# Optimization experiments

Hardware: AMD Instinct MI355X
Metric: run time of the kernel (lower is better)

Reference implementation:

```python
import jax, jax.numpy as jnp
import numpy as np

B, S, HID = 2, 2048, 2048
H, DH = 16, 128
SCALE = 1.0 / np.sqrt(DH)


def setup_inputs() -> dict:
    key = jax.random.key(0)
    ks = jax.random.split(key, 5)
    std = 1.0 / np.sqrt(HID)
    return {
        "x": jax.random.normal(ks[0], (B, S, HID), dtype=jnp.float32),
        "wq": jax.random.normal(ks[1], (HID, HID), dtype=jnp.float32) * std,
        "wk": jax.random.normal(ks[2], (HID, HID), dtype=jnp.float32) * std,
        "wv": jax.random.normal(ks[3], (HID, HID), dtype=jnp.float32) * std,
        "wo": jax.random.normal(ks[4], (HID, HID), dtype=jnp.float32) * std,
    }


def reference(x, wq, wk, wv, wo):
    # nn.Linear(h, h, bias=False): y = x @ W^T
    q = (x @ wq.T).reshape(B, S, H, DH).transpose(0, 2, 1, 3)  # [B,H,S,Dh]
    k = (x @ wk.T).reshape(B, S, H, DH).transpose(0, 2, 1, 3)
    v = (x @ wv.T).reshape(B, S, H, DH).transpose(0, 2, 1, 3)
    scores = jnp.einsum("bhsd,bhtd->bhst", q, k) * SCALE  # [B,H,S,S]
    attn = jax.nn.softmax(scores.astype(jnp.float32), axis=-1).astype(q.dtype)
    # dropout p=0.0 (eval): identity
    out = jnp.einsum("bhst,bhtd->bhsd", attn, v)  # [B,H,S,Dh]
    out = out.transpose(0, 2, 1, 3).reshape(B, S, HID)
    return out @ wo.T
```

## Files before the change

kernel.cpp:

```cpp
#include <hip/hip_runtime.h>
#include <hip/hip_bf16.h>
#include <stdint.h>

typedef __attribute__((ext_vector_type(8))) short short8;
typedef __attribute__((ext_vector_type(4))) short short4v;
typedef __attribute__((ext_vector_type(4))) float f32x4;
typedef __attribute__((ext_vector_type(4))) unsigned int uint4v;

static __device__ __forceinline__ ushort f2bf(float f) {
    uint32_t u = __builtin_bit_cast(uint32_t, f);
    uint32_t r = (u + 0x7FFFu + ((u >> 16) & 1u)) >> 16;
    return (ushort)r;
}

static __device__ __forceinline__ uint32_t cvt_pk_bf16(float lo, float hi) {
    uint32_t d;
    asm("v_cvt_pk_bf16_f32 %0, %1, %2" : "=v"(d) : "v"(lo), "v"(hi));
    return d;
}

static __device__ __forceinline__ void async_copy16(const void* g, void* l) {
    __builtin_amdgcn_global_load_lds(
        (const __attribute__((address_space(1))) uint32_t*)g,
        (__attribute__((address_space(3))) uint32_t*)l, 16, 0, 0);
}

#define TR16(P3, IMM)                                                        \
    ({                                                                       \
        short4v _d;                                                          \
        asm volatile("ds_read_b64_tr_b16 %0, %1 offset:" #IMM                \
                     : "=v"(_d) : "v"(P3));                                  \
        _d;                                                                  \
    })

#define CAT8(a, b) __builtin_shufflevector(a, b, 0, 1, 2, 3, 4, 5, 6, 7)

__global__ __launch_bounds__(256) void cast_kernel(const float* __restrict__ in,
                                                   ushort* __restrict__ out, int n4) {
    int i = blockIdx.x * 256 + threadIdx.x;
    if (i >= n4) return;
    float4 v = reinterpret_cast<const float4*>(in)[i];
    uint2 o;
    o.x = cvt_pk_bf16(v.x, v.y);
    o.y = cvt_pk_bf16(v.z, v.w);
    reinterpret_cast<uint2*>(out)[i] = o;
}

__global__ __launch_bounds__(256) void cast3_kernel(const float* __restrict__ a,
                                                    const float* __restrict__ b,
                                                    const float* __restrict__ c,
                                                    ushort* __restrict__ out, int n4each) {
    int i = blockIdx.x * 256 + threadIdx.x;
    int which = i / n4each;
    int j = i - which * n4each;
    const float* src = which == 0 ? a : (which == 1 ? b : c);
    if (which > 2) return;
    float4 v = reinterpret_cast<const float4*>(src)[j];
    uint2 o;
    o.x = cvt_pk_bf16(v.x, v.y);
    o.y = cvt_pk_bf16(v.z, v.w);
    reinterpret_cast<uint2*>(out)[i] = o;
}

static __device__ __forceinline__ void store_val(float* C, size_t idx, float v) { C[idx] = v; }
static __device__ __forceinline__ void store_val(ushort* C, size_t idx, float v) { C[idx] = f2bf(v); }

template <typename OutT>
__global__ __launch_bounds__(256) void gemm_bt_kernel(const ushort* __restrict__ A,
                                                      const ushort* __restrict__ B,
                                                      OutT* __restrict__ C,
                                                      int M, int N, int K) {
    __shared__ __align__(16) ushort As[128 * 32];
    __shared__ __align__(16) ushort Bs[128 * 32];
    const int tid = threadIdx.x;
    const int w = tid >> 6, lane = tid & 63;
    const int fr = lane & 15, fq = lane >> 4;
    const int wr = w >> 1, wc = w & 1;
    const int bpn = N >> 7;
    const int which = blockIdx.x / bpn;
    const int row0 = blockIdx.y * 128;
    const int gcol0 = blockIdx.x * 128;
    const int col0 = gcol0 - which * N;
    OutT* Cw = C + (size_t)which * M * N;

    const int srow = tid >> 2;
    const int scol = (tid & 3) * 8;
    const ushort* ga0 = A + (size_t)(row0 + srow) * K + scol;
    const ushort* ga1 = A + (size_t)(row0 + 64 + srow) * K + scol;
    const ushort* gb0 = B + (size_t)(gcol0 + srow) * K + scol;
    const ushort* gb1 = B + (size_t)(gcol0 + 64 + srow) * K + scol;
    ushort* la0 = &As[(w * 64) * 8];
    ushort* la1 = &As[(256 + w * 64) * 8];
    ushort* lb0 = &Bs[(w * 64) * 8];
    ushort* lb1 = &Bs[(256 + w * 64) * 8];

    f32x4 acc[4][4];
#pragma unroll
    for (int m = 0; m < 4; ++m)
#pragma unroll
        for (int n = 0; n < 4; ++n) acc[m][n] = f32x4{0.f, 0.f, 0.f, 0.f};

    for (int kt = 0; kt < K; kt += 32) {
        __syncthreads();
        async_copy16(ga0 + kt, la0);
        async_copy16(ga1 + kt, la1);
        async_copy16(gb0 + kt, lb0);
        async_copy16(gb1 + kt, lb1);
        __syncthreads();
        short8 af[4], bfr[4];
#pragma unroll
        for (int m = 0; m < 4; ++m)
            af[m] = *(const short8*)&As[(wr * 64 + m * 16 + fr) * 32 + fq * 8];
#pragma unroll
        for (int n = 0; n < 4; ++n)
            bfr[n] = *(const short8*)&Bs[(wc * 64 + n * 16 + fr) * 32 + fq * 8];
#pragma unroll
        for (int m = 0; m < 4; ++m)
#pragma unroll
            for (int n = 0; n < 4; ++n)
                acc[m][n] = __builtin_amdgcn_mfma_f32_16x16x32_bf16(af[m], bfr[n], acc[m][n], 0, 0, 0);
    }

#pragma unroll
    for (int m = 0; m < 4; ++m) {
        const int grow = row0 + wr * 64 + m * 16 + fq * 4;
#pragma unroll
        for (int n = 0; n < 4; ++n) {
            const int gcol = col0 + wc * 64 + n * 16 + fr;
#pragma unroll
            for (int r = 0; r < 4; ++r)
                store_val(Cw, (size_t)(grow + r) * N + gcol, acc[m][n][r]);
        }
    }
}

__global__ __launch_bounds__(512) void attn_kernel(const ushort* __restrict__ Q,
                                                   const ushort* __restrict__ K,
                                                   const ushort* __restrict__ V,
                                                   ushort* __restrict__ O,
                                                   int S, int HID, float scale) {
    __shared__ __align__(16) ushort Ks[64 * 128];
    __shared__ __align__(16) ushort Vs[64 * 128];

    const int tid = threadIdx.x, w = tid >> 6, lane = tid & 63;
    const int fr = lane & 15, fq = lane >> 4;
    const int qt = blockIdx.x, h = blockIdx.y, b = blockIdx.z;
    const size_t rs = (size_t)HID;
    const int qr0 = qt * 128 + w * 16;
    const float c1 = scale * 1.4426950408889634f;

    short8 qf[4];
    {
        const ushort* qp = Q + ((size_t)(b * S) + qr0 + fr) * rs + h * 128 + fq * 8;
#pragma unroll
        for (int ks = 0; ks < 4; ++ks) qf[ks] = *(const short8*)(qp + ks * 32);
    }

    f32x4 of[8];
#pragma unroll
    for (int n = 0; n < 8; ++n) of[n] = f32x4{0.f, 0.f, 0.f, 0.f};
    float m2 = -1e30f;
    float l = 0.f;

    const ushort* Kb = K + (size_t)(b * S) * rs + h * 128;
    const ushort* Vb = V + (size_t)(b * S) * rs + h * 128;

    size_t koff[2];
#pragma unroll
    for (int j = 0; j < 2; ++j) {
        int row = j * 32 + w * 4 + (lane >> 4);
        int colb = ((lane & 15) * 16) ^ ((row & 7) << 4);
        koff[j] = (size_t)row * rs + (colb >> 1);
    }
    size_t voff[2];
#pragma unroll
    for (int j = 0; j < 2; ++j) {
        int L = j * 64 + w * 8 + (lane >> 3);
        int kv = (L >> 3) * 4 + ((lane >> 1) & 3);
        int dh = (L & 7) * 16 + (lane & 1) * 8;
        voff[j] = (size_t)kv * rs + dh;
    }

    const __attribute__((address_space(3))) ushort* vb3 =
        (const __attribute__((address_space(3))) ushort*)((const char*)Vs + fq * 2048 + fr * 8);

    const int srcA = fr + 16 * ((2 * fq) & 3);
    const int srcB = fr + 16 * ((2 * fq + 1) & 3);
    const int par = fq >> 1;

    const int nt = S / 64;
    for (int t = 0; t < nt; ++t) {
        __syncthreads();
        const ushort* kt0 = Kb + (size_t)t * 64 * rs;
        const ushort* vt0 = Vb + (size_t)t * 64 * rs;
#pragma unroll
        for (int j = 0; j < 2; ++j)
            async_copy16(kt0 + koff[j], &Ks[j * 4096 + w * 512]);
#pragma unroll
        for (int j = 0; j < 2; ++j)
            async_copy16(vt0 + voff[j], &Vs[j * 4096 + w * 512]);
        __syncthreads();

        f32x4 sf[4];
        __builtin_amdgcn_s_setprio(1);
#pragma unroll
        for (int kc = 0; kc < 4; ++kc) {
            f32x4 s = f32x4{0.f, 0.f, 0.f, 0.f};
#pragma unroll
            for (int ks = 0; ks < 4; ++ks) {
                int row = kc * 16 + fr;
                int pb = (row * 256 + ks * 64 + fq * 16) ^ ((row & 7) << 4);
                short8 kf = *(const short8*)((const char*)Ks + pb);
                s = __builtin_amdgcn_mfma_f32_16x16x32_bf16(kf, qf[ks], s, 0, 0, 0);
            }
            sf[kc] = s;
        }
        __builtin_amdgcn_s_setprio(0);

        float pm = fmaxf(fmaxf(fmaxf(sf[0][0], sf[0][1]), fmaxf(sf[0][2], sf[0][3])),
                         fmaxf(fmaxf(sf[1][0], sf[1][1]), fmaxf(sf[1][2], sf[1][3])));
        pm = fmaxf(pm, fmaxf(fmaxf(fmaxf(sf[2][0], sf[2][1]), fmaxf(sf[2][2], sf[2][3])),
                             fmaxf(fmaxf(sf[3][0], sf[3][1]), fmaxf(sf[3][2], sf[3][3]))));
        pm = fmaxf(pm, __shfl_xor(pm, 16));
        pm = fmaxf(pm, __shfl_xor(pm, 32));
        float pm2 = pm * c1;
        const bool noresc = __all(pm2 - m2 <= 8.0f);
        float sc = 1.0f;
        if (!noresc) {
            float m2new = fmaxf(m2, pm2);
            sc = exp2f(m2 - m2new);
            m2 = m2new;
        }
        float rsum = 0.f;
#pragma unroll
        for (int kc = 0; kc < 4; ++kc)
#pragma unroll
            for (int r = 0; r < 4; ++r) {
                float p = exp2f(sf[kc][r] * c1 - m2);
                sf[kc][r] = p;
                rsum += p;
            }
        rsum += __shfl_xor(rsum, 16);
        rsum += __shfl_xor(rsum, 32);
        if (noresc) {
            l = l + rsum;
        } else {
            l = l * sc + rsum;
#pragma unroll
            for (int n = 0; n < 8; ++n) {
                f32x4 o = of[n];
                o[0] *= sc; o[1] *= sc; o[2] *= sc; o[3] *= sc;
                of[n] = o;
            }
        }

        uint32_t cpk[4][2];
#pragma unroll
        for (int kc = 0; kc < 4; ++kc)
#pragma unroll
            for (int hh = 0; hh < 2; ++hh)
                cpk[kc][hh] = cvt_pk_bf16(sf[kc][2 * hh], sf[kc][2 * hh + 1]);

        __builtin_amdgcn_s_setprio(1);
        {
            uint32_t eA0 = __shfl(cpk[0][0], srcA), eA1 = __shfl(cpk[0][1], srcA);
            uint32_t oA0 = __shfl(cpk[1][0], srcA), oA1 = __shfl(cpk[1][1], srcA);
            uint32_t eB0 = __shfl(cpk[0][0], srcB), eB1 = __shfl(cpk[0][1], srcB);
            uint32_t oB0 = __shfl(cpk[1][0], srcB), oB1 = __shfl(cpk[1][1], srcB);
            uint4v pd;
            pd[0] = par ? oA0 : eA0; pd[1] = par ? oA1 : eA1;
            pd[2] = par ? oB0 : eB0; pd[3] = par ? oB1 : eB1;
            short8 pf = __builtin_bit_cast(short8, pd);
            {
                short4v a0 = TR16(vb3, 0),    b0 = TR16(vb3, 1024);
                short4v a1 = TR16(vb3, 128),  b1 = TR16(vb3, 1152);
                short4v a2 = TR16(vb3, 256),  b2 = TR16(vb3, 1280);
                short4v a3 = TR16(vb3, 384),  b3 = TR16(vb3, 1408);
                asm volatile("s_waitcnt lgkmcnt(0)" ::: "memory");
                __builtin_amdgcn_sched_barrier(0);
                of[0] = __builtin_amdgcn_mfma_f32_16x16x32_bf16(CAT8(a0, b0), pf, of[0], 0, 0, 0);
                of[1] = __builtin_amdgcn_mfma_f32_16x16x32_bf16(CAT8(a1, b1), pf, of[1], 0, 0, 0);
                of[2] = __builtin_amdgcn_mfma_f32_16x16x32_bf16(CAT8(a2, b2), pf, of[2], 0, 0, 0);
                of[3] = __builtin_amdgcn_mfma_f32_16x16x32_bf16(CAT8(a3, b3), pf, of[3], 0, 0, 0);
            }
            {
                short4v a0 = TR16(vb3, 512),  b0 = TR16(vb3, 1536);
                short4v a1 = TR16(vb3, 640),  b1 = TR16(vb3, 1664);
                short4v a2 = TR16(vb3, 768),  b2 = TR16(vb3, 1792);
                short4v a3 = TR16(vb3, 896),  b3 = TR16(vb3, 1920);
                asm volatile("s_waitcnt lgkmcnt(0)" ::: "memory");
                __builtin_amdgcn_sched_barrier(0);
                of[4] = __builtin_amdgcn_mfma_f32_16x16x32_bf16(CAT8(a0, b0), pf, of[4], 0, 0, 0);
                of[5] = __builtin_amdgcn_mfma_f32_16x16x32_bf16(CAT8(a1, b1), pf, of[5], 0, 0, 0);
                of[6] = __builtin_amdgcn_mfma_f32_16x16x32_bf16(CAT8(a2, b2), pf, of[6], 0, 0, 0);
                of[7] = __builtin_amdgcn_mfma_f32_16x16x32_bf16(CAT8(a3, b3), pf, of[7], 0, 0, 0);
            }
        }
        {
            uint32_t eA0 = __shfl(cpk[2][0], srcA), eA1 = __shfl(cpk[2][1], srcA);
            uint32_t oA0 = __shfl(cpk[3][0], srcA), oA1 = __shfl(cpk[3][1], srcA);
            uint32_t eB0 = __shfl(cpk[2][0], srcB), eB1 = __shfl(cpk[2][1], srcB);
            uint32_t oB0 = __shfl(cpk[3][0], srcB), oB1 = __shfl(cpk[3][1], srcB);
            uint4v pd;
            pd[0] = par ? oA0 : eA0; pd[1] = par ? oA1 : eA1;
            pd[2] = par ? oB0 : eB0; pd[3] = par ? oB1 : eB1;
            short8 pf = __builtin_bit_cast(short8, pd);
            {
                short4v a0 = TR16(vb3, 8192), b0 = TR16(vb3, 9216);
                short4v a1 = TR16(vb3, 8320), b1 = TR16(vb3, 9344);
                short4v a2 = TR16(vb3, 8448), b2 = TR16(vb3, 9472);
                short4v a3 = TR16(vb3, 8576), b3 = TR16(vb3, 9600);
                asm volatile("s_waitcnt lgkmcnt(0)" ::: "memory");
                __builtin_amdgcn_sched_barrier(0);
                of[0] = __builtin_amdgcn_mfma_f32_16x16x32_bf16(CAT8(a0, b0), pf, of[0], 0, 0, 0);
                of[1] = __builtin_amdgcn_mfma_f32_16x16x32_bf16(CAT8(a1, b1), pf, of[1], 0, 0, 0);
                of[2] = __builtin_amdgcn_mfma_f32_16x16x32_bf16(CAT8(a2, b2), pf, of[2], 0, 0, 0);
                of[3] = __builtin_amdgcn_mfma_f32_16x16x32_bf16(CAT8(a3, b3), pf, of[3], 0, 0, 0);
            }
            {
                short4v a0 = TR16(vb3, 8704), b0 = TR16(vb3, 9728);
                short4v a1 = TR16(vb3, 8832), b1 = TR16(vb3, 9856);
                short4v a2 = TR16(vb3, 8960), b2 = TR16(vb3, 9984);
                short4v a3 = TR16(vb3, 9088), b3 = TR16(vb3, 10112);
                asm volatile("s_waitcnt lgkmcnt(0)" ::: "memory");
                __builtin_amdgcn_sched_barrier(0);
                of[4] = __builtin_amdgcn_mfma_f32_16x16x32_bf16(CAT8(a0, b0), pf, of[4], 0, 0, 0);
                of[5] = __builtin_amdgcn_mfma_f32_16x16x32_bf16(CAT8(a1, b1), pf, of[5], 0, 0, 0);
                of[6] = __builtin_amdgcn_mfma_f32_16x16x32_bf16(CAT8(a2, b2), pf, of[6], 0, 0, 0);
                of[7] = __builtin_amdgcn_mfma_f32_16x16x32_bf16(CAT8(a3, b3), pf, of[7], 0, 0, 0);
            }
        }
        __builtin_amdgcn_s_setprio(0);
    }

    float inv = 1.f / l;
    ushort* ob = O + ((size_t)(b * S) + qr0 + fr) * rs + h * 128 + fq * 4;
#pragma unroll
    for (int n = 0; n < 8; ++n) {
        uint2 o2;
        o2.x = cvt_pk_bf16(of[n][0] * inv, of[n][1] * inv);
        o2.y = cvt_pk_bf16(of[n][2] * inv, of[n][3] * inv);
        *reinterpret_cast<uint2*>(ob + n * 16) = o2;
    }
}

extern "C" void kernel_launch(void* const* d_in, const int* in_sizes, int n_in,
                              void* d_out, int out_size, void* d_ws, size_t ws_size,
                              hipStream_t stream) {
    constexpr int B = 2, S = 2048, HID = 2048, H = 16;
    constexpr int M = B * S;
    const float scale = 0.08838834764831845f;

    const float* x  = (const float*)d_in[0];
    const float* wq = (const float*)d_in[1];
    const float* wk = (const float*)d_in[2];
    const float* wv = (const float*)d_in[3];
    const float* wo = (const float*)d_in[4];
    float* out = (float*)d_out;

    char* ws = (char*)d_ws;
    ushort* xb  = (ushort*)(ws);
    ushort* wqb = (ushort*)(ws + 16777216);
    ushort* qb  = (ushort*)(ws + 41943040);
    ushort* kb  = (ushort*)(ws + 58720256);
    ushort* vb  = (ushort*)(ws + 75497472);

    const int XN = M * HID;
    const int WN = HID * HID;

    cast_kernel<<<XN / 4 / 256, 256, 0, stream>>>(x, xb, XN / 4);
    cast3_kernel<<<3 * WN / 4 / 256, 256, 0, stream>>>(wq, wk, wv, wqb, WN / 4);

    dim3 gq(3 * HID / 128, M / 128);
    gemm_bt_kernel<ushort><<<gq, 256, 0, stream>>>(xb, wqb, qb, M, HID, HID);

    dim3 ga(S / 128, H, B);
    attn_kernel<<<ga, 512, 0, stream>>>(qb, kb, vb, xb, S, HID, scale);

    cast_kernel<<<WN / 4 / 256, 256, 0, stream>>>(wo, wqb, WN / 4);
    dim3 gg(HID / 128, M / 128);
    gemm_bt_kernel<float><<<gg, 256, 0, stream>>>(xb, wqb, out, M, HID, HID);
}
```

Measured before the change: 338.8 us.

## Use 256x256-tile pipelined GEMM kernel for fused QKV projection

Adds a new bf16 GEMM kernel with 256x256 output tiles per 512-thread block. It uses a 4-deep ring of async global-to-LDS copies with swizzled layout and vmcnt-based waits, and raises wave priority around the MFMA block. The fused QKV projection switches from the 128x128-tile kernel to this one, aiming for more operand reuse and better overlap of loads with MFMA work. The trade-offs are 128KB of LDS per block and a much smaller grid, 384 blocks, which risks load imbalance across CUs.

```diff
diff --git a/kernel.cpp b/kernel.cpp
--- a/kernel.cpp
+++ b/kernel.cpp
@@ -130,6 +130,94 @@
 #pragma unroll
             for (int r = 0; r < 4; ++r)
                 store_val(Cw, (size_t)(grow + r) * N + gcol, acc[m][n][r]);
+        }
+    }
+}
+
+__global__ __launch_bounds__(512, 2) void gemm256_kernel(const ushort* __restrict__ A,
+                                                         const ushort* __restrict__ B,
+                                                         ushort* __restrict__ C,
+                                                         int M, int N, int K) {
+    __shared__ __align__(16) char smem[131072];
+    const int tid = threadIdx.x, w = tid >> 6, lane = tid & 63;
+    const int fr = lane & 15, fq = lane >> 4;
+    const int wm = w >> 2, wn = w & 3;
+    const int bpn = N >> 8;
+    const int which = blockIdx.x / bpn;
+    const int row0 = blockIdx.y * 256;
+    const int gcol0 = blockIdx.x * 256;
+    const int col0 = gcol0 - which * N;
+    ushort* Cw = C + (size_t)which * M * N;
+
+    const int lo = ((tid & 7) ^ ((tid >> 3) & 7)) << 4;
+    const int r0p = ((tid >> 3) << 1) + (lo >> 6);
+    const int colE = (lo & 63) >> 1;
+    const ushort* Ap0 = A + (size_t)(row0 + r0p) * K + colE;
+    const ushort* Ap1 = A + (size_t)(row0 + 128 + r0p) * K + colE;
+    const ushort* Bp0 = B + (size_t)(gcol0 + r0p) * K + colE;
+    const ushort* Bp1 = B + (size_t)(gcol0 + 128 + r0p) * K + colE;
+
+    char* aregs = smem;
+    char* bregs = smem + 65536;
+    const int wbyte = w * 1024;
+
+    auto stageH = [&](int h) {
+        const int kc = (h >> 1) * 64 + (h & 1) * 32;
+        char* ar = aregs + (h & 3) * 16384;
+        char* br = bregs + (h & 3) * 16384;
+        async_copy16(Ap0 + kc, ar + wbyte);
+        async_copy16(Ap1 + kc, ar + 8192 + wbyte);
+        async_copy16(Bp0 + kc, br + wbyte);
+        async_copy16(Bp1 + kc, br + 8192 + wbyte);
+    };
+
+    const int swz = ((fr & 1) * 64 + fq * 16) ^ (((fr >> 1) & 7) << 4);
+    const int aBase = (wm * 64 + (fr >> 1)) * 128 + swz;
+    const int bBase = (wn * 32 + (fr >> 1)) * 128 + swz;
+
+    f32x4 acc[8][4];
+#pragma unroll
+    for (int m = 0; m < 8; ++m)
+#pragma unroll
+        for (int n = 0; n < 4; ++n) acc[m][n] = f32x4{0.f, 0.f, 0.f, 0.f};
+
+    const int nH = K >> 5;
+    stageH(0); stageH(1); stageH(2);
+    asm volatile("s_waitcnt vmcnt(8)\n\ts_barrier" ::: "memory");
+
+    for (int i = 0; i < nH; ++i) {
+        if (i + 3 < nH) stageH(i + 3);
+        const char* ar = aregs + (i & 3) * 16384 + aBase;
+        const char* br = bregs + (i & 3) * 16384 + bBase;
+        short8 af[8], bf[4];
+#pragma unroll
+        for (int m = 0; m < 8; ++m) af[m] = *(const short8*)(ar + m * 1024);
+#pragma unroll
+        for (int n = 0; n < 4; ++n) bf[n] = *(const short8*)(br + n * 1024);
+        __builtin_amdgcn_s_setprio(1);
+#pragma unroll
+        for (int m = 0; m < 8; ++m)
+#pragma unroll
+            for (int n = 0; n < 4; ++n)
+                acc[m][n] = __builtin_amdgcn_mfma_f32_16x16x32_bf16(af[m], bf[n], acc[m][n], 0, 0, 0);
+        __builtin_amdgcn_s_setprio(0);
+        if (i < nH - 3)
+            asm volatile("s_waitcnt vmcnt(8)\n\ts_barrier" ::: "memory");
+        else if (i == nH - 3)
+            asm volatile("s_waitcnt vmcnt(4)\n\ts_barrier" ::: "memory");
+        else if (i == nH - 2)
+            asm volatile("s_waitcnt vmcnt(0)\n\ts_barrier" ::: "memory");
+    }
+
+#pragma unroll
+    for (int m = 0; m < 8; ++m) {
+        const int grow = row0 + wm * 128 + m * 16 + fq * 4;
+#pragma unroll
+        for (int n = 0; n < 4; ++n) {
+            const int gcol = col0 + wn * 64 + n * 16 + fr;
+#pragma unroll
+            for (int r2 = 0; r2 < 4; ++r2)
+                Cw[(size_t)(grow + r2) * N + gcol] = f2bf(acc[m][n][r2]);
         }
     }
 }
@@ -371,8 +459,8 @@
     cast_kernel<<<XN / 4 / 256, 256, 0, stream>>>(x, xb, XN / 4);
     cast3_kernel<<<3 * WN / 4 / 256, 256, 0, stream>>>(wq, wk, wv, wqb, WN / 4);
 
-    dim3 gq(3 * HID / 128, M / 128);
-    gemm_bt_kernel<ushort><<<gq, 256, 0, stream>>>(xb, wqb, qb, M, HID, HID);
+    dim3 gq(3 * HID / 256, M / 256);
+    gemm256_kernel<<<gq, 512, 0, stream>>>(xb, wqb, qb, M, HID, HID);
 
     dim3 ga(S / 128, H, B);
     attn_kernel<<<ga, 512, 0, stream>>>(qb, kb, vb, xb, S, HID, scale);
```

After: 326.1 us. 1.04x faster.
